# Optimization experiments

Hardware: AMD Instinct MI355X
Metric: run time of the kernel (lower is better)

The kernel has to match this reference:

```python
import jax, jax.numpy as jnp
from jax import lax
import numpy as np

B = 512      # instances
C = 64       # cases (segments)
HID = 1024
ATT = 128


def _conv(x, w, b):
    # torch Conv2d(kernel=5, padding=2), NCHW / OIHW layout
    y = lax.conv_general_dilated(x, w, (1, 1), [(2, 2), (2, 2)],
                                 dimension_numbers=('NCHW', 'OIHW', 'NCHW'))
    return y + b[None, :, None, None]


def _pool(x):
    # MaxPool2d(2)
    return lax.reduce_window(x, -jnp.inf, lax.max, (1, 1, 2, 2), (1, 1, 2, 2), 'VALID')


def setup_inputs() -> dict:
    key = jax.random.key(0)
    ks = jax.random.split(key, 20)

    def rn(k, shape, scale=0.05):
        return jax.random.normal(k, shape, dtype=jnp.float32) * scale

    inp = {
        'data': jax.random.normal(ks[0], (B, 3, 128, 128), dtype=jnp.float32),
        'case_ids': jnp.sort(jax.random.randint(ks[1], (B,), 0, C, dtype=jnp.int32)),
    }
    chans = [(3, 8), (8, 16), (16, 32), (32, 64), (64, 128)]
    for i, (ci, co) in enumerate(chans):
        inp[f'conv_w{i + 1}'] = rn(ks[2 + 2 * i], (co, ci, 5, 5))
        inp[f'conv_b{i + 1}'] = jnp.zeros((co,), jnp.float32)
    inp['fc_w'] = rn(ks[12], (HID, 128 * 4 * 4), 0.02)
    inp['fc_b'] = jnp.zeros((HID,), jnp.float32)
    inp['att_w1'] = rn(ks[13], (ATT, HID), 0.02)
    inp['att_b1'] = jnp.zeros((ATT,), jnp.float32)
    inp['att_w2'] = rn(ks[14], (1, ATT), 0.02)
    inp['att_b2'] = jnp.zeros((1,), jnp.float32)
    inp['clf_w'] = rn(ks[15], (1, HID), 0.02)
    inp['clf_b'] = jnp.zeros((1,), jnp.float32)
    return inp


def reference(data, case_ids, conv_w1, conv_b1, conv_w2, conv_b2, conv_w3, conv_b3,
              conv_w4, conv_b4, conv_w5, conv_b5, fc_w, fc_b,
              att_w1, att_b1, att_w2, att_b2, clf_w, clf_b):
    x = data
    for w, b in ((conv_w1, conv_b1), (conv_w2, conv_b2), (conv_w3, conv_b3),
                 (conv_w4, conv_b4), (conv_w5, conv_b5)):
        x = jax.nn.relu(_pool(_conv(x, w, b)))
    emb = x.reshape(x.shape[0], -1) @ fc_w.T + fc_b          # (B, HID)

    # --- segment (per-case) attention pooling, vectorized over all cases ---
    logits = (jnp.tanh(emb @ att_w1.T + att_b1) @ att_w2.T + att_b2)[:, 0]  # (B,)
    seg_max = jax.ops.segment_max(logits, case_ids, num_segments=C)
    seg_max = jnp.where(jnp.isfinite(seg_max), seg_max, 0.0)  # guard empty segments
    e = jnp.exp(logits - lax.stop_gradient(seg_max)[case_ids])
    denom = jax.ops.segment_sum(e, case_ids, num_segments=C)
    wgt = e / denom[case_ids]                                  # segment softmax
    aggr = jax.ops.segment_sum(wgt[:, None] * emb, case_ids, num_segments=C)  # (C, HID)

    # --- classifier ---
    return jax.nn.sigmoid(aggr @ clf_w.T + clf_b)              # (C, 1)
```

## Files before the change

kernel.cpp:

```cpp
#include <hip/hip_runtime.h>
#include <hip/hip_bf16.h>
#include <math.h>

#define BATCH 512
#define NSEG  64
#define HID   1024
#define ATT   128

typedef __attribute__((ext_vector_type(8))) __bf16 bf16x8;
typedef __attribute__((ext_vector_type(4))) __bf16 bf16x4;
typedef __attribute__((ext_vector_type(4))) float  f32x4;

__global__ void wconv1_k(const float* __restrict__ w, __bf16* __restrict__ wt) {
    int t = blockIdx.x * 256 + threadIdx.x;
    if (t >= 2048) return;
    int j = t & 7, m = (t >> 3) & 15, k8 = t >> 7;
    int k = k8 * 8 + j, tap = k >> 2, ci = k & 3;
    float v = 0.f;
    if (m < 8 && ci < 3 && tap < 25) v = w[(m * 3 + ci) * 25 + tap];
    wt[t] = (__bf16)v;
}

__global__ __launch_bounds__(256) void conv1_mfma_k(
    const float* __restrict__ in, const __bf16* __restrict__ Wt,
    const float* __restrict__ bias, __bf16* __restrict__ out) {
    constexpr int W  = 128;
    constexpr int R  = 4;
    constexpr int RP = R + 4;
    constexpr int WP = W + 4;
    constexpr int CSTR = R * W + 4;

    __shared__ __align__(16) __bf16 xs[RP * WP * 4];
    __shared__ float cs[8 * CSTR];

    const int tid = threadIdx.x;
    const int b   = blockIdx.x >> 5;
    const int y0  = (blockIdx.x & 31) * R;
    const float* inb = in + (size_t)b * 3 * 16384;

    if (tid < RP * 4) {
        int r = tid >> 2, s = tid & 3;
        int c = (s < 2) ? s : (128 + s);
        *(bf16x4*)(xs + (r * WP + c) * 4) = (bf16x4){};
    }
    {
        int r  = tid >> 5;
        int g  = tid & 31;
        int gy = y0 + r - 2;
        int c0 = g * 4;
        bf16x8 lo = {}, hi = {};
        if ((unsigned)gy < 128u) {
            const float* p = inb + (size_t)gy * 128 + c0;
            float4 a = *(const float4*)(p);
            float4 q = *(const float4*)(p + 16384);
            float4 c = *(const float4*)(p + 32768);
            lo[0] = (__bf16)a.x; lo[1] = (__bf16)q.x; lo[2] = (__bf16)c.x;
            lo[4] = (__bf16)a.y; lo[5] = (__bf16)q.y; lo[6] = (__bf16)c.y;
            hi[0] = (__bf16)a.z; hi[1] = (__bf16)q.z; hi[2] = (__bf16)c.z;
            hi[4] = (__bf16)a.w; hi[5] = (__bf16)q.w; hi[6] = (__bf16)c.w;
        }
        *(bf16x8*)(xs + (r * WP + c0 + 2) * 4)     = lo;
        *(bf16x8*)(xs + (r * WP + c0 + 2) * 4 + 8) = hi;
    }
    __syncthreads();

    const int lane = tid & 63, wave = tid >> 6;
    const int quad = lane >> 4, l15 = lane & 15;
    constexpr int F = 8;

    int pbase[F];
    f32x4 acc[F];
#pragma unroll
    for (int f = 0; f < F; ++f) {
        pbase[f] = ((wave + 2) * WP + f * 16 + l15 + 2) * 8;
        acc[f] = f32x4{0.f, 0.f, 0.f, 0.f};
    }
    const char* xsb = (const char*)xs;

#pragma unroll
    for (int kt = 0; kt < 4; ++kt) {
        int k8 = kt * 4 + quad;
        int tap0 = k8 * 2, tap1 = tap0 + 1;
        int t0 = tap0 < 25 ? tap0 : 0;
        int t1 = tap1 < 25 ? tap1 : 0;
        int s0 = ((t0 / 5 - 2) * WP + (t0 % 5 - 2)) * 8;
        int s1 = ((t1 / 5 - 2) * WP + (t1 % 5 - 2)) * 8;
        bf16x8 av = *(const bf16x8*)(Wt + ((size_t)k8 * 16 + l15) * 8);
#pragma unroll
        for (int f = 0; f < F; ++f) {
            bf16x4 b0 = *(const bf16x4*)(xsb + pbase[f] + s0);
            bf16x4 b1 = *(const bf16x4*)(xsb + pbase[f] + s1);
            bf16x8 bv = __builtin_shufflevector(b0, b1, 0, 1, 2, 3, 4, 5, 6, 7);
            acc[f] = __builtin_amdgcn_mfma_f32_16x16x32_bf16(av, bv, acc[f], 0, 0, 0);
        }
    }

#pragma unroll
    for (int f = 0; f < F; ++f) {
        int pl = wave * 128 + f * 16 + l15;
#pragma unroll
        for (int r = 0; r < 4; ++r) {
            int m = quad * 4 + r;
            if (m < 8) cs[m * CSTR + pl] = acc[f][r];
        }
    }
    __syncthreads();

    {
        int oi  = tid >> 1;
        int cog = (tid & 1) * 4;
        int oy  = oi >> 6, ox = oi & 63;
        int pl0 = oy * 2 * 128 + ox * 2;
        float4 b4 = *(const float4*)(bias + cog);
        bf16x4 ov;
#pragma unroll
        for (int i = 0; i < 4; ++i) {
            int cr = cog + i;
            float v0 = cs[cr * CSTR + pl0],       v1 = cs[cr * CSTR + pl0 + 1];
            float v2 = cs[cr * CSTR + pl0 + 128], v3 = cs[cr * CSTR + pl0 + 129];
            float m = fmaxf(fmaxf(v0, v1), fmaxf(v2, v3)) + ((const float*)&b4)[i];
            ov[i] = (__bf16)fmaxf(m, 0.f);
        }
        size_t ob = ((size_t)b * 4096 + (size_t)(y0 / 2 + oy) * 64 + ox) * 8 + cog;
        *(bf16x4*)(out + ob) = ov;
    }
}

template<int Ci, int Co>
__global__ void wconv_k(const float* __restrict__ w, __bf16* __restrict__ wt) {
    const int n = 25 * Ci * Co;
    int t = blockIdx.x * 256 + threadIdx.x;
    if (t >= n) return;
    int j  = t & 7;
    int t2 = t >> 3;
    int co = t2 % Co;
    int k8 = t2 / Co;
    int k  = k8 * 8 + j;
    int tap = k / Ci, ci = k % Ci;
    int kh = tap / 5, kw = tap % 5;
    wt[t] = (__bf16)w[((co * Ci + ci) * 25) + kh * 5 + kw];
}

__global__ void wfc_k(const float* __restrict__ w, __bf16* __restrict__ wt) {
    int t = blockIdx.x * 256 + threadIdx.x;
    int j  = t & 7;
    int t2 = t >> 3;
    int o  = t2 & 1023;
    int k8 = t2 >> 10;
    wt[t] = (__bf16)w[(size_t)o * 2048 + k8 * 8 + j];
}

template<int Ci, int Co, int H, int RB, int IMGS, int OUTMODE>
__global__ __launch_bounds__(256) void conv2d_mfma_k(
    const __bf16* __restrict__ X, const __bf16* __restrict__ Wt,
    const float* __restrict__ bias, void* __restrict__ outp) {
    constexpr int W   = H;
    constexpr int PW  = W + 4;
    constexpr int PR  = RB + 4;
    constexpr int PIX = RB * W;
    constexpr int P   = IMGS * PIX;
    constexpr int SE  = Ci + (Ci >= 16 ? 8 : 0);
    constexpr int SB  = SE * 2;
    constexpr int K   = 25 * Ci;
    constexpr int KTF = K / 32;
    constexpr int FW  = P / 64;
    constexpr int PP  = P / 4;
    constexpr int OW  = W / 2;
    constexpr int CSTR = P + 1;
    constexpr int C8  = Ci / 8;
    constexpr int BPI = H / RB;

    constexpr int XS_B = IMGS * PR * PW * SB;
    constexpr int CS_B = 16 * CSTR * 4;
    constexpr int SM_B = XS_B > CS_B ? XS_B : CS_B;
    __shared__ __align__(16) char smem[SM_B];
    __bf16* xs = (__bf16*)smem;
    float*  cs = (float*)smem;

    const int tid = threadIdx.x;
    const int b0  = (blockIdx.x / BPI) * IMGS;
    const int y0  = (blockIdx.x % BPI) * RB;
    const int co0 = blockIdx.y * 16;

    constexpr int NSLOT = IMGS * PR * PW * C8;
    for (int i = tid; i < NSLOT; i += 256) {
        int s   = i % C8;
        int t2  = i / C8;
        int pc  = t2 % PW;
        int t3  = t2 / PW;
        int pr  = t3 % PR;
        int img = t3 / PR;
        int gy  = y0 + pr - 2;
        int gx  = pc - 2;
        bf16x8 v = {};
        if ((unsigned)gy < (unsigned)H && (unsigned)gx < (unsigned)W)
            v = *(const bf16x8*)(X + (((size_t)(b0 + img) * H + gy) * W + gx) * Ci + s * 8);
        *(bf16x8*)((char*)xs + ((size_t)(img * PR + pr) * PW + pc) * SB + s * 16) = v;
    }
    __syncthreads();

    const int lane = tid & 63, wave = tid >> 6;
    const int quad = lane >> 4, l15 = lane & 15;

    int pbase[FW];
    f32x4 acc[FW];
#pragma unroll
    for (int f = 0; f < FW; ++f) {
        int pos = (wave * FW + f) * 16 + l15;
        int img = pos / PIX;
        int r   = (pos & (PIX - 1)) / W;
        int c   = pos & (W - 1);
        pbase[f] = (img * PR + (r + 2)) * PW * SB + (c + 2) * SB;
        acc[f] = f32x4{0.f, 0.f, 0.f, 0.f};
    }
    const char* xsb = (const char*)smem;
    const bf16x8 BZ = {};

    auto body = [&](int kt, bool mask) {
        int k8  = kt * 4 + quad;
        int kk  = k8 * 8;
        int kok = 1;
        if (mask) { kok = kk < K; if (!kok) { k8 = 0; kk = 0; } }
        int tap = kk / Ci, cio = kk % Ci;
        int dy  = tap / 5 - 2, dx = tap % 5 - 2;
        int shift = (dy * PW + dx) * SB + cio * 2;
        bf16x8 av = *(const bf16x8*)(Wt + ((size_t)k8 * Co + co0 + l15) * 8);
#pragma unroll
        for (int f = 0; f < FW; ++f) {
            bf16x8 bv = *(const bf16x8*)(xsb + pbase[f] + shift);
            if (mask && !kok) bv = BZ;
            acc[f] = __builtin_amdgcn_mfma_f32_16x16x32_bf16(av, bv, acc[f], 0, 0, 0);
        }
    };
#pragma unroll
    for (int kt = 0; kt < KTF; ++kt) body(kt, false);
    if constexpr (K % 32 != 0) body(KTF, true);

    __syncthreads();
#pragma unroll
    for (int f = 0; f < FW; ++f) {
        int pl = (wave * FW + f) * 16 + l15;
#pragma unroll
        for (int r = 0; r < 4; ++r) cs[(quad * 4 + r) * CSTR + pl] = acc[f][r];
    }
    __syncthreads();

    constexpr int SLOTS = PP * 4;
    if (tid < SLOTS) {
        int opos = tid >> 2;
        int cog  = (tid & 3) * 4;
        constexpr int PPI = PIX / 4;
        int img  = opos / PPI;
        int rest = opos & (PPI - 1);
        int oyl  = rest / OW;
        int oxl  = rest & (OW - 1);
        int pl0  = img * PIX + (oyl * 2) * W + oxl * 2;
        int bb   = b0 + img;
        int oy   = (y0 >> 1) + oyl;
        float4 b4 = *(const float4*)(bias + co0 + cog);
        float mv[4];
#pragma unroll
        for (int i = 0; i < 4; ++i) {
            int cr = cog + i;
            float v0 = cs[cr * CSTR + pl0],     v1 = cs[cr * CSTR + pl0 + 1];
            float v2 = cs[cr * CSTR + pl0 + W], v3 = cs[cr * CSTR + pl0 + W + 1];
            float m = fmaxf(fmaxf(v0, v1), fmaxf(v2, v3)) + ((const float*)&b4)[i];
            mv[i] = fmaxf(m, 0.f);
        }
        if (OUTMODE == 1) {
#pragma unroll
            for (int i = 0; i < 4; ++i)
                ((__bf16*)outp)[(size_t)bb * 2048 + (co0 + cog + i) * 16 + oy * 4 + oxl] =
                    (__bf16)mv[i];
        } else {
            bf16x4 ov;
#pragma unroll
            for (int i = 0; i < 4; ++i) ov[i] = (__bf16)mv[i];
            *(bf16x4*)((__bf16*)outp +
                (((size_t)bb * (H / 2) + oy) * OW + oxl) * Co + co0 + cog) = ov;
        }
    }
}

__global__ __launch_bounds__(256) void fc_mfma_k(
    const __bf16* __restrict__ Xb, const __bf16* __restrict__ Wfc,
    const float* __restrict__ bias, float* __restrict__ emb) {
    const int tid  = threadIdx.x;
    const int lane = tid & 63, wave = tid >> 6;
    const int quad = lane >> 4, l15 = lane & 15;
    const int n0   = blockIdx.x * 128;
    const int co0  = blockIdx.y * 16;

    int n[2];
    f32x4 acc[2];
#pragma unroll
    for (int f = 0; f < 2; ++f) {
        n[f] = n0 + wave * 32 + f * 16 + l15;
        acc[f] = f32x4{0.f, 0.f, 0.f, 0.f};
    }

#pragma unroll 4
    for (int kt = 0; kt < 64; ++kt) {
        int k8 = kt * 4 + quad;
        bf16x8 av = *(const bf16x8*)(Wfc + ((size_t)k8 * 1024 + co0 + l15) * 8);
#pragma unroll
        for (int f = 0; f < 2; ++f) {
            bf16x8 bv = *(const bf16x8*)(Xb + (size_t)n[f] * 2048 + k8 * 8);
            acc[f] = __builtin_amdgcn_mfma_f32_16x16x32_bf16(av, bv, acc[f], 0, 0, 0);
        }
    }

    float4 b4 = *(const float4*)(bias + co0 + quad * 4);
#pragma unroll
    for (int f = 0; f < 2; ++f) {
        f32x4 v = acc[f];
        v[0] += b4.x; v[1] += b4.y; v[2] += b4.z; v[3] += b4.w;
        *(f32x4*)(emb + (size_t)n[f] * 1024 + co0 + quad * 4) = v;
    }
}

__global__ __launch_bounds__(128) void attention_k(
    const float* __restrict__ emb, const float* __restrict__ w1,
    const float* __restrict__ b1, const float* __restrict__ w2,
    const float* __restrict__ b2, float* __restrict__ logits) {
    const int b = blockIdx.x;
    const int j = threadIdx.x;
    __shared__ float es[HID];
    for (int k = j; k < HID; k += 128) es[k] = emb[(size_t)b * HID + k];
    __syncthreads();

    float s = b1[j];
    const float* wr = w1 + (size_t)j * HID;
    for (int k = 0; k < HID; k += 4) {
        float4 wv = *(const float4*)(wr + k);
        float4 ev = *(const float4*)(es + k);
        s += wv.x * ev.x + wv.y * ev.y + wv.z * ev.z + wv.w * ev.w;
    }
    float v = tanhf(s) * w2[j];
#pragma unroll
    for (int off = 32; off > 0; off >>= 1) v += __shfl_down(v, off);
    __shared__ float wsum[2];
    if ((j & 63) == 0) wsum[j >> 6] = v;
    __syncthreads();
    if (j == 0) logits[b] = wsum[0] + wsum[1] + b2[0];
}

__global__ __launch_bounds__(256) void segment_k(
    const float* __restrict__ emb, const float* __restrict__ logits,
    const int* __restrict__ cid, const float* __restrict__ clf_w,
    const float* __restrict__ clf_b, float* __restrict__ out) {
    const int c = blockIdx.x;
    const int t = threadIdx.x;
    __shared__ int cids[BATCH];
    __shared__ float red[256];
    for (int i = t; i < BATCH; i += 256) cids[i] = cid[i];
    __syncthreads();

    float lm = -1e30f;
    for (int b = t; b < BATCH; b += 256)
        if (cids[b] == c) lm = fmaxf(lm, logits[b]);
    red[t] = lm; __syncthreads();
    for (int s = 128; s > 0; s >>= 1) {
        if (t < s) red[t] = fmaxf(red[t], red[t + s]);
        __syncthreads();
    }
    float smax = red[0]; __syncthreads();

    float ls = 0.f;
    for (int b = t; b < BATCH; b += 256)
        if (cids[b] == c) ls += expf(logits[b] - smax);
    red[t] = ls; __syncthreads();
    for (int s = 128; s > 0; s >>= 1) {
        if (t < s) red[t] += red[t + s];
        __syncthreads();
    }
    float denom = red[0]; __syncthreads();
    float inv = (denom > 0.f) ? 1.f / denom : 0.f;

    const int h0 = t * 4;
    float g0 = 0.f, g1 = 0.f, g2 = 0.f, g3 = 0.f;
    for (int b = 0; b < BATCH; ++b) {
        if (cids[b] == c) {
            float wgt = expf(logits[b] - smax) * inv;
            float4 ev = *(const float4*)(emb + (size_t)b * HID + h0);
            g0 = fmaf(wgt, ev.x, g0);
            g1 = fmaf(wgt, ev.y, g1);
            g2 = fmaf(wgt, ev.z, g2);
            g3 = fmaf(wgt, ev.w, g3);
        }
    }
    float4 cw = *(const float4*)(clf_w + h0);
    float ca = g0 * cw.x + g1 * cw.y + g2 * cw.z + g3 * cw.w;
    red[t] = ca; __syncthreads();
    for (int s = 128; s > 0; s >>= 1) {
        if (t < s) red[t] += red[t + s];
        __syncthreads();
    }
    if (t == 0) out[c] = 1.f / (1.f + expf(-(red[0] + clf_b[0])));
}

extern "C" void kernel_launch(void* const* d_in, const int* in_sizes, int n_in,
                              void* d_out, int out_size, void* d_ws, size_t ws_size,
                              hipStream_t stream) {
    const float* data = (const float*)d_in[0];
    const int*   cid  = (const int*)d_in[1];
    const float* cw1 = (const float*)d_in[2],  * cb1 = (const float*)d_in[3];
    const float* cw2 = (const float*)d_in[4],  * cb2 = (const float*)d_in[5];
    const float* cw3 = (const float*)d_in[6],  * cb3 = (const float*)d_in[7];
    const float* cw4 = (const float*)d_in[8],  * cb4 = (const float*)d_in[9];
    const float* cw5 = (const float*)d_in[10], * cb5 = (const float*)d_in[11];
    const float* fcw = (const float*)d_in[12], * fcb = (const float*)d_in[13];
    const float* aw1 = (const float*)d_in[14], * ab1 = (const float*)d_in[15];
    const float* aw2 = (const float*)d_in[16], * ab2 = (const float*)d_in[17];
    const float* clw = (const float*)d_in[18], * clb = (const float*)d_in[19];
    float* out = (float*)d_out;

    char* wsb = (char*)d_ws;
    __bf16* x1  = (__bf16*)(wsb);
    __bf16* x2  = (__bf16*)(wsb + 33554432);
    __bf16* x3  = (__bf16*)(wsb + 50331648);
    __bf16* x4  = (__bf16*)(wsb + 58720256);
    __bf16* x5b = (__bf16*)(wsb + 62914560);
    float*  emb = (float*) (wsb + 65011712);
    float*  lg  = (float*) (wsb + 67108864);
    __bf16* wt2 = (__bf16*)(wsb + 67110912);
    __bf16* wt3 = (__bf16*)(wsb + 67117312);
    __bf16* wt4 = (__bf16*)(wsb + 67142912);
    __bf16* wt5 = (__bf16*)(wsb + 67245312);
    __bf16* wfc = (__bf16*)(wsb + 67654912);
    __bf16* wt1 = (__bf16*)(wsb + 71849216);

    wconv1_k<<<8, 256, 0, stream>>>(cw1, wt1);
    wconv_k<8,  16 ><<<(3200   + 255) / 256, 256, 0, stream>>>(cw2, wt2);
    wconv_k<16, 32 ><<<(12800  + 255) / 256, 256, 0, stream>>>(cw3, wt3);
    wconv_k<32, 64 ><<<(51200  + 255) / 256, 256, 0, stream>>>(cw4, wt4);
    wconv_k<64, 128><<<(204800 + 255) / 256, 256, 0, stream>>>(cw5, wt5);
    wfc_k<<<2097152 / 256, 256, 0, stream>>>(fcw, wfc);

    conv1_mfma_k<<<16384, 256, 0, stream>>>(data, wt1, cb1, x1);

    conv2d_mfma_k<8,  16,  64, 4,  1, 0><<<dim3(512 * 16, 1), 256, 0, stream>>>(x1, wt2, cb2, x2);
    conv2d_mfma_k<16, 32,  32, 8,  1, 0><<<dim3(512 * 4,  2), 256, 0, stream>>>(x2, wt3, cb3, x3);
    conv2d_mfma_k<32, 64,  16, 16, 1, 0><<<dim3(512,      4), 256, 0, stream>>>(x3, wt4, cb4, x4);
    conv2d_mfma_k<64, 128, 8,  8,  2, 1><<<dim3(256,      8), 256, 0, stream>>>(x4, wt5, cb5, x5b);

    fc_mfma_k<<<dim3(4, 64), 256, 0, stream>>>(x5b, wfc, fcb, emb);
    attention_k<<<BATCH, 128, 0, stream>>>(emb, aw1, ab1, aw2, ab2, lg);
    segment_k<<<NSEG, 256, 0, stream>>>(emb, lg, cid, clw, clb, out);
}
```

Measured before the change: 433.7 us.

## Compute all output channels per conv block, pool in registers, MFMA attention

Each conv block now loops over every output-channel tile, so the input halo staged in shared memory is loaded once rather than once per channel group. Pixel-to-lane mapping is reorganised so the 2x2 max-pool runs with lane shuffles in registers, removing the shared-memory staging pass and its extra barriers. The attention projection is rewritten as a bf16 MFMA GEMM over 16-instance tiles, converting fp32 inputs on the fly. The cost is many more accumulator registers per thread (FW x NCOT tiles), which can lower occupancy or cause spills, and only 8 blocks for attention.

```diff
diff --git a/kernel.cpp b/kernel.cpp
--- a/kernel.cpp
+++ b/kernel.cpp
@@ -154,33 +154,26 @@
 __global__ __launch_bounds__(256) void conv2d_mfma_k(
     const __bf16* __restrict__ X, const __bf16* __restrict__ Wt,
     const float* __restrict__ bias, void* __restrict__ outp) {
-    constexpr int W   = H;
-    constexpr int PW  = W + 4;
-    constexpr int PR  = RB + 4;
-    constexpr int PIX = RB * W;
-    constexpr int P   = IMGS * PIX;
-    constexpr int SE  = Ci + (Ci >= 16 ? 8 : 0);
-    constexpr int SB  = SE * 2;
-    constexpr int K   = 25 * Ci;
-    constexpr int KTF = K / 32;
-    constexpr int FW  = P / 64;
-    constexpr int PP  = P / 4;
-    constexpr int OW  = W / 2;
-    constexpr int CSTR = P + 1;
-    constexpr int C8  = Ci / 8;
-    constexpr int BPI = H / RB;
-
-    constexpr int XS_B = IMGS * PR * PW * SB;
-    constexpr int CS_B = 16 * CSTR * 4;
-    constexpr int SM_B = XS_B > CS_B ? XS_B : CS_B;
-    __shared__ __align__(16) char smem[SM_B];
-    __bf16* xs = (__bf16*)smem;
-    float*  cs = (float*)smem;
+    constexpr int W    = H;
+    constexpr int PW   = W + 4;
+    constexpr int PR   = RB + 4;
+    constexpr int PIX  = RB * W;
+    constexpr int P    = IMGS * PIX;
+    constexpr int SE   = Ci + (Ci >= 16 ? 8 : 0);
+    constexpr int SB   = SE * 2;
+    constexpr int K    = 25 * Ci;
+    constexpr int KTF  = K / 32;
+    constexpr int FW   = P / 64;
+    constexpr int NCOT = Co / 16;
+    constexpr int C8   = Ci / 8;
+    constexpr int BPI  = H / RB;
+    constexpr int OW   = W / 2;
+
+    __shared__ __align__(16) char smem[IMGS * PR * PW * SB];
 
     const int tid = threadIdx.x;
     const int b0  = (blockIdx.x / BPI) * IMGS;
     const int y0  = (blockIdx.x % BPI) * RB;
-    const int co0 = blockIdx.y * 16;
 
     constexpr int NSLOT = IMGS * PR * PW * C8;
     for (int i = tid; i < NSLOT; i += 256) {
@@ -195,7 +188,7 @@
         bf16x8 v = {};
         if ((unsigned)gy < (unsigned)H && (unsigned)gx < (unsigned)W)
             v = *(const bf16x8*)(X + (((size_t)(b0 + img) * H + gy) * W + gx) * Ci + s * 8);
-        *(bf16x8*)((char*)xs + ((size_t)(img * PR + pr) * PW + pc) * SB + s * 16) = v;
+        *(bf16x8*)(smem + ((size_t)(img * PR + pr) * PW + pc) * SB + s * 16) = v;
     }
     __syncthreads();
 
@@ -203,81 +196,105 @@
     const int quad = lane >> 4, l15 = lane & 15;
 
     int pbase[FW];
-    f32x4 acc[FW];
-#pragma unroll
-    for (int f = 0; f < FW; ++f) {
-        int pos = (wave * FW + f) * 16 + l15;
-        int img = pos / PIX;
-        int r   = (pos & (PIX - 1)) / W;
-        int c   = pos & (W - 1);
-        pbase[f] = (img * PR + (r + 2)) * PW * SB + (c + 2) * SB;
-        acc[f] = f32x4{0.f, 0.f, 0.f, 0.f};
-    }
-    const char* xsb = (const char*)smem;
+    f32x4 acc[FW][NCOT];
+    int rg = 0, ch = 0, gbase = 0, img5 = 0;
+    if constexpr (W >= 16) {
+        constexpr int C16 = W / 16;
+        ch = wave % C16;
+        rg = wave / C16;
+#pragma unroll
+        for (int f = 0; f < FW; ++f) {
+            int row = rg * FW + f;
+            pbase[f] = ((row + 2) * PW + ch * 16 + l15 + 2) * SB;
+        }
+    } else {
+        img5  = wave >> 1;
+        gbase = (wave & 1) * FW;
+#pragma unroll
+        for (int f = 0; f < FW; ++f) {
+            int g    = gbase + f;
+            int row0 = 2 * g + (l15 >> 3);
+            pbase[f] = ((img5 * PR + row0 + 2) * PW + (l15 & 7) + 2) * SB;
+        }
+    }
+#pragma unroll
+    for (int f = 0; f < FW; ++f)
+#pragma unroll
+        for (int c = 0; c < NCOT; ++c) acc[f][c] = f32x4{0.f, 0.f, 0.f, 0.f};
+
     const bf16x8 BZ = {};
-
-    auto body = [&](int kt, bool mask) {
-        int k8  = kt * 4 + quad;
-        int kk  = k8 * 8;
-        int kok = 1;
+    auto kstep = [&](int kt, bool mask) {
+        int k8 = kt * 4 + quad;
+        int kk = k8 * 8;
+        bool kok = true;
         if (mask) { kok = kk < K; if (!kok) { k8 = 0; kk = 0; } }
         int tap = kk / Ci, cio = kk % Ci;
-        int dy  = tap / 5 - 2, dx = tap % 5 - 2;
+        int dy = tap / 5 - 2, dx = tap % 5 - 2;
         int shift = (dy * PW + dx) * SB + cio * 2;
-        bf16x8 av = *(const bf16x8*)(Wt + ((size_t)k8 * Co + co0 + l15) * 8);
+        bf16x8 bv[FW];
 #pragma unroll
         for (int f = 0; f < FW; ++f) {
-            bf16x8 bv = *(const bf16x8*)(xsb + pbase[f] + shift);
-            if (mask && !kok) bv = BZ;
-            acc[f] = __builtin_amdgcn_mfma_f32_16x16x32_bf16(av, bv, acc[f], 0, 0, 0);
+            bv[f] = *(const bf16x8*)(smem + pbase[f] + shift);
+            if (mask && !kok) bv[f] = BZ;
+        }
+#pragma unroll
+        for (int c = 0; c < NCOT; ++c) {
+            bf16x8 av = *(const bf16x8*)(Wt + ((size_t)k8 * Co + c * 16 + l15) * 8);
+#pragma unroll
+            for (int f = 0; f < FW; ++f)
+                acc[f][c] = __builtin_amdgcn_mfma_f32_16x16x32_bf16(av, bv[f], acc[f][c], 0, 0, 0);
         }
     };
-#pragma unroll
-    for (int kt = 0; kt < KTF; ++kt) body(kt, false);
-    if constexpr (K % 32 != 0) body(KTF, true);
-
-    __syncthreads();
-#pragma unroll
-    for (int f = 0; f < FW; ++f) {
-        int pl = (wave * FW + f) * 16 + l15;
-#pragma unroll
-        for (int r = 0; r < 4; ++r) cs[(quad * 4 + r) * CSTR + pl] = acc[f][r];
-    }
-    __syncthreads();
-
-    constexpr int SLOTS = PP * 4;
-    if (tid < SLOTS) {
-        int opos = tid >> 2;
-        int cog  = (tid & 3) * 4;
-        constexpr int PPI = PIX / 4;
-        int img  = opos / PPI;
-        int rest = opos & (PPI - 1);
-        int oyl  = rest / OW;
-        int oxl  = rest & (OW - 1);
-        int pl0  = img * PIX + (oyl * 2) * W + oxl * 2;
-        int bb   = b0 + img;
-        int oy   = (y0 >> 1) + oyl;
-        float4 b4 = *(const float4*)(bias + co0 + cog);
-        float mv[4];
-#pragma unroll
-        for (int i = 0; i < 4; ++i) {
-            int cr = cog + i;
-            float v0 = cs[cr * CSTR + pl0],     v1 = cs[cr * CSTR + pl0 + 1];
-            float v2 = cs[cr * CSTR + pl0 + W], v3 = cs[cr * CSTR + pl0 + W + 1];
-            float m = fmaxf(fmaxf(v0, v1), fmaxf(v2, v3)) + ((const float*)&b4)[i];
-            mv[i] = fmaxf(m, 0.f);
-        }
-        if (OUTMODE == 1) {
-#pragma unroll
-            for (int i = 0; i < 4; ++i)
-                ((__bf16*)outp)[(size_t)bb * 2048 + (co0 + cog + i) * 16 + oy * 4 + oxl] =
-                    (__bf16)mv[i];
-        } else {
-            bf16x4 ov;
-#pragma unroll
-            for (int i = 0; i < 4; ++i) ov[i] = (__bf16)mv[i];
-            *(bf16x4*)((__bf16*)outp +
-                (((size_t)bb * (H / 2) + oy) * OW + oxl) * Co + co0 + cog) = ov;
+#pragma unroll 2
+    for (int kt = 0; kt < KTF; ++kt) kstep(kt, false);
+    if constexpr (K % 32 != 0) kstep(KTF, true);
+
+    if constexpr (W >= 16) {
+#pragma unroll
+        for (int fp = 0; fp < FW / 2; ++fp) {
+            int f0  = 2 * fp;
+            int row = rg * FW + f0;
+            int oy  = (y0 + row) >> 1;
+            int ox  = (ch * 16 + l15) >> 1;
+            bool on = (l15 & 1) == 0;
+#pragma unroll
+            for (int c = 0; c < NCOT; ++c) {
+                float4 bb = *(const float4*)(bias + c * 16 + quad * 4);
+                bf16x4 ov;
+#pragma unroll
+                for (int r = 0; r < 4; ++r) {
+                    float v0 = acc[f0][c][r];
+                    float h0 = fmaxf(v0, __shfl_xor(v0, 1));
+                    float v1 = acc[f0 + 1][c][r];
+                    float h1 = fmaxf(v1, __shfl_xor(v1, 1));
+                    float m  = fmaxf(h0, h1) + ((const float*)&bb)[r];
+                    ov[r] = (__bf16)fmaxf(m, 0.f);
+                }
+                if (on)
+                    *(bf16x4*)((__bf16*)outp +
+                        (((size_t)b0 * (H / 2) + oy) * OW + ox) * Co + c * 16 + quad * 4) = ov;
+            }
+        }
+    } else {
+#pragma unroll
+        for (int f = 0; f < FW; ++f) {
+            int g   = gbase + f;
+            bool on = ((l15 & 1) == 0) && (l15 < 8);
+            int ox  = (l15 & 7) >> 1;
+#pragma unroll
+            for (int c = 0; c < NCOT; ++c) {
+                float4 bb = *(const float4*)(bias + c * 16 + quad * 4);
+#pragma unroll
+                for (int r = 0; r < 4; ++r) {
+                    float v  = acc[f][c][r];
+                    float h  = fmaxf(v, __shfl_xor(v, 1));
+                    float m2 = fmaxf(h, __shfl_xor(h, 8));
+                    float m  = fmaxf(m2 + ((const float*)&bb)[r], 0.f);
+                    if (on)
+                        ((__bf16*)outp)[(size_t)(b0 + img5) * 2048 +
+                            (c * 16 + quad * 4 + r) * 16 + g * 4 + ox] = (__bf16)m;
+                }
+            }
         }
     }
 }
@@ -319,30 +336,48 @@
     }
 }
 
-__global__ __launch_bounds__(128) void attention_k(
+__device__ inline bf16x8 cvt8(const float* __restrict__ p) {
+    float4 a = *(const float4*)p, b = *(const float4*)(p + 4);
+    bf16x8 v;
+    v[0] = (__bf16)a.x; v[1] = (__bf16)a.y; v[2] = (__bf16)a.z; v[3] = (__bf16)a.w;
+    v[4] = (__bf16)b.x; v[5] = (__bf16)b.y; v[6] = (__bf16)b.z; v[7] = (__bf16)b.w;
+    return v;
+}
+
+__global__ __launch_bounds__(256) void att_mfma_k(
     const float* __restrict__ emb, const float* __restrict__ w1,
     const float* __restrict__ b1, const float* __restrict__ w2,
     const float* __restrict__ b2, float* __restrict__ logits) {
-    const int b = blockIdx.x;
-    const int j = threadIdx.x;
-    __shared__ float es[HID];
-    for (int k = j; k < HID; k += 128) es[k] = emb[(size_t)b * HID + k];
-    __syncthreads();
-
-    float s = b1[j];
-    const float* wr = w1 + (size_t)j * HID;
-    for (int k = 0; k < HID; k += 4) {
-        float4 wv = *(const float4*)(wr + k);
-        float4 ev = *(const float4*)(es + k);
-        s += wv.x * ev.x + wv.y * ev.y + wv.z * ev.z + wv.w * ev.w;
-    }
-    float v = tanhf(s) * w2[j];
-#pragma unroll
-    for (int off = 32; off > 0; off >>= 1) v += __shfl_down(v, off);
-    __shared__ float wsum[2];
-    if ((j & 63) == 0) wsum[j >> 6] = v;
-    __syncthreads();
-    if (j == 0) logits[b] = wsum[0] + wsum[1] + b2[0];
+    const int tid = threadIdx.x, lane = tid & 63, wave = tid >> 6;
+    const int quad = lane >> 4, l15 = lane & 15;
+    const int n = (blockIdx.x * 4 + wave) * 16 + l15;
+
+    f32x4 acc[8];
+#pragma unroll
+    for (int t = 0; t < 8; ++t) acc[t] = f32x4{0.f, 0.f, 0.f, 0.f};
+
+    for (int kt = 0; kt < 32; ++kt) {
+        int k8 = kt * 4 + quad;
+        bf16x8 bv = cvt8(emb + (size_t)n * 1024 + k8 * 8);
+#pragma unroll
+        for (int t = 0; t < 8; ++t) {
+            bf16x8 av = cvt8(w1 + (size_t)(t * 16 + l15) * 1024 + k8 * 8);
+            acc[t] = __builtin_amdgcn_mfma_f32_16x16x32_bf16(av, bv, acc[t], 0, 0, 0);
+        }
+    }
+
+    float sum = 0.f;
+#pragma unroll
+    for (int t = 0; t < 8; ++t) {
+#pragma unroll
+        for (int r = 0; r < 4; ++r) {
+            int j = t * 16 + quad * 4 + r;
+            sum += tanhf(acc[t][r] + b1[j]) * w2[j];
+        }
+    }
+    sum += __shfl_xor(sum, 16);
+    sum += __shfl_xor(sum, 32);
+    if (quad == 0) logits[n] = sum + b2[0];
 }
 
 __global__ __launch_bounds__(256) void segment_k(
@@ -439,12 +474,12 @@
 
     conv1_mfma_k<<<16384, 256, 0, stream>>>(data, wt1, cb1, x1);
 
-    conv2d_mfma_k<8,  16,  64, 4,  1, 0><<<dim3(512 * 16, 1), 256, 0, stream>>>(x1, wt2, cb2, x2);
-    conv2d_mfma_k<16, 32,  32, 8,  1, 0><<<dim3(512 * 4,  2), 256, 0, stream>>>(x2, wt3, cb3, x3);
-    conv2d_mfma_k<32, 64,  16, 16, 1, 0><<<dim3(512,      4), 256, 0, stream>>>(x3, wt4, cb4, x4);
-    conv2d_mfma_k<64, 128, 8,  8,  2, 1><<<dim3(256,      8), 256, 0, stream>>>(x4, wt5, cb5, x5b);
+    conv2d_mfma_k<8,  16,  64, 8,  1, 0><<<4096, 256, 0, stream>>>(x1, wt2, cb2, x2);
+    conv2d_mfma_k<16, 32,  32, 8,  1, 0><<<2048, 256, 0, stream>>>(x2, wt3, cb3, x3);
+    conv2d_mfma_k<32, 64,  16, 16, 1, 0><<<512,  256, 0, stream>>>(x3, wt4, cb4, x4);
+    conv2d_mfma_k<64, 128, 8,  8,  2, 1><<<256,  256, 0, stream>>>(x4, wt5, cb5, x5b);
 
     fc_mfma_k<<<dim3(4, 64), 256, 0, stream>>>(x5b, wfc, fcb, emb);
-    attention_k<<<BATCH, 128, 0, stream>>>(emb, aw1, ab1, aw2, ab2, lg);
+    att_mfma_k<<<8, 256, 0, stream>>>(emb, aw1, ab1, aw2, ab2, lg);
     segment_k<<<NSEG, 256, 0, stream>>>(emb, lg, cid, clw, clb, out);
 }
```

Measured after the change: 575.7 us. +32.7%, slower.
